# Kernel tuning notes

Hardware: AMD Instinct MI355X
Metric: run time of the kernel (lower is better)

The kernel has to match this reference:

```python
import jax, jax.numpy as jnp
import numpy as np
from jax import lax

# 4D convolution via lax.conv_general_dilated (supports N spatial dims natively)
# Layout: x is (N, C, T, U, V, W); weight is (O, I, kT, kU, kV, kW)

def conv4d(x, w, b):
    dn = lax.conv_dimension_numbers(x.shape, w.shape, ('NCTUVW', 'OITUVW', 'NCTUVW'))
    y = lax.conv_general_dilated(x, w, window_strides=(1, 1, 1, 1), padding='SAME',
                                 dimension_numbers=dn)
    return y + b[None, :, None, None, None, None]


def setup_inputs() -> dict:
    key = jax.random.key(0)
    k0, k1, k2, k3, k4 = jax.random.split(key, 5)
    B, C_in, C_hid, C_out = 2, 64, 128, 64
    T, D, H, W = 4, 16, 32, 32
    K = 3  # kernel size per dim (stmode 'C' -> (3,3,3,3))
    x = jax.random.normal(k0, (B, C_in, T, D, H, W), dtype=jnp.float32)
    scale1 = 1.0 / np.sqrt(C_in * K ** 4)
    scale2 = 1.0 / np.sqrt(C_hid * K ** 4)
    w1 = jax.random.normal(k1, (C_hid, C_in, K, K, K, K), dtype=jnp.float32) * scale1
    b1 = jax.random.normal(k2, (C_hid,), dtype=jnp.float32) * scale1
    w2 = jax.random.normal(k3, (C_out, C_hid, K, K, K, K), dtype=jnp.float32) * scale2
    b2 = jax.random.normal(k4, (C_out,), dtype=jnp.float32) * scale2
    return {"x": x, "w1": w1, "b1": b1, "w2": w2, "b2": b2}


def reference(x, w1, b1, w2, b2):
    # conv1 -> ReLU -> (dropout p=0 is identity) -> conv2 -> (dropout identity)
    h = jax.nn.relu(conv4d(x, w1, b1))
    return conv4d(h, w2, b2)
```

## Files before the change

### kernel.cpp

```cpp
#include <hip/hip_runtime.h>


using bf16x8 = __attribute__((ext_vector_type(8))) __bf16;
using f32x16 = __attribute__((ext_vector_type(16))) float;
using f32x4  = __attribute__((ext_vector_type(4))) float;

typedef __attribute__((address_space(1))) const void as1_void;
typedef __attribute__((address_space(3))) void as3_void;
__device__ __forceinline__ void gload_lds16(const void* g, void* l) {
    __builtin_amdgcn_global_load_lds((as1_void*)g, (as3_void*)l, 16, 0, 0);
}

__global__ __launch_bounds__(256) void cvt_x(const float* __restrict__ x,
                                             __bf16* __restrict__ x_t) {
    __shared__ float lt[64][65];
    const int nb = blockIdx.y;
    const int p0 = blockIdx.x * 64;
    const int tu = p0 >> 10;
    const float* src = x + (size_t)nb * 64 * 65536;
    __bf16* dst = x_t + (size_t)nb * 65536 * 64;
    #pragma unroll
    for (int i = 0; i < 16; ++i) {
        int idx = i * 256 + threadIdx.x;
        int c = idx >> 6, p = idx & 63;
        lt[c][p] = src[(size_t)c * 65536 + p0 + p];
    }
    __syncthreads();
    #pragma unroll
    for (int i = 0; i < 16; ++i) {
        int idx = i * 256 + threadIdx.x;
        int c = idx >> 6, pl = idx & 63;
        int p = p0 + pl;
        int v = (p >> 5) & 31, w = p & 31;
        dst[(size_t)(tu * 32 + v) * 2048 + (c >> 3) * 256 + w * 8 + (c & 7)] =
            (__bf16)lt[c][pl];
    }
}

template <int CIN>
__global__ __launch_bounds__(256) void cvt_w(const float* __restrict__ w,
                                             __bf16* __restrict__ wt) {
    constexpr int COUT = 8192 / CIN;
    constexpr int LOGC = (CIN == 64) ? 7 : 6;
    const int tap = blockIdx.x;
    __bf16* dst = wt + (size_t)tap * 8192;
    #pragma unroll
    for (int it = 0; it < 32; ++it) {
        const int i  = it * 256 + threadIdx.x;
        const int cl = i & 15;
        const int o  = (i >> 4) & (COUT - 1);
        const int kg = i >> (4 + LOGC);
        dst[i] = (__bf16)w[(size_t)(o * CIN + kg * 16 + cl) * 81 + tap];
    }
}

template <int CIN, int COUT, int GM, int GN, int WPEU, bool RELU>
__global__ __launch_bounds__(256, WPEU) void conv4d_mfma(
    const __bf16* __restrict__ in_t,
    const __bf16* __restrict__ wt,
    const float* __restrict__ bias,
    __bf16* __restrict__ out_bf,
    float* __restrict__ out_f)
{
    constexpr int KST   = CIN / 16;
    constexpr int UNITS = CIN / 32;
    constexpr int LOGU  = (UNITS == 2) ? 1 : 2;
    constexpr int VSPAN = GM * 4;
    constexpr int VGB   = (VSPAN == 4) ? 3 : 2;
    constexpr int ROWS  = VSPAN + 2;
    constexpr int SLOTS = ROWS * 136;
    constexpr int RNDS  = (SLOTS + 255) / 256;
    constexpr int BUFB  = SLOTS * 16;

    __shared__ __bf16 tile[2 * SLOTS * 8];

    const int tid  = threadIdx.x;
    const int lane = tid & 63;
    const int l31  = lane & 31;
    const int hl   = lane >> 5;
    const int wv   = tid >> 6;
    const int gmi  = (GM == 2) ? (wv >> 1) : 0;
    const int gni  = (GM == 2) ? (wv & 1) : wv;

    const int bid = blockIdx.x;
    const int xcd = bid & 7;
    const int s0  = bid >> 3;
    const int u   = xcd * 2 + (s0 & 1);
    const int vg  = (s0 >> 1) & ((1 << VGB) - 1);
    const int t   = (s0 >> (1 + VGB)) & 3;
    const int nb  = (s0 >> (3 + VGB)) & 1;
    const int v0  = vg * VSPAN;
    const int pbase = ((t * 16 + u) * 32 + v0) * 32;

    const __bf16* inb = in_t + (size_t)nb * 65536 * CIN;

    int goff[RNDS];
    #pragma unroll
    for (int r = 0; r < RNDS; ++r) {
        const int slot = r * 256 + tid;
        const int row  = slot / 136;
        const int rem  = slot - row * 136;
        const int chunk = rem / 34;
        const int wp   = rem - chunk * 34;
        const int v_in = v0 - 1 + row;
        const int w_in = wp - 1;
        const bool ok = (slot < SLOTS) && ((unsigned)v_in < 32u) &&
                        ((unsigned)w_in < 32u);
        goff[r] = ok ? (v_in * (CIN * 32) + chunk * 256 + w_in * 8) : -1;
    }

    #pragma unroll
    for (int r = 0; r < RNDS; ++r) {
        const int slot = r * 256 + tid;
        if (slot < SLOTS && goff[r] < 0) {
            *(uint4*)((char*)tile + slot * 16) = make_uint4(0u, 0u, 0u, 0u);
            *(uint4*)((char*)tile + BUFB + slot * 16) = make_uint4(0u, 0u, 0u, 0u);
        }
    }

    const int lane_base = gmi * 4 * 136 + hl * 34 + l31;
    const bf16x8* tile16 = (const bf16x8*)tile;

    const __bf16* wlane = wt + ((size_t)(gni * 32 + l31)) * 16 + hl * 8;

    int sb[9], tb0[9], nst = 0;
    #pragma unroll
    for (int kt = 0; kt < 3; ++kt) {
        const int t_in = t + kt - 1;
        if ((unsigned)t_in >= 4u) continue;
        #pragma unroll
        for (int ku = 0; ku < 3; ++ku) {
            const int u_in = u + ku - 1;
            if ((unsigned)u_in >= 16u) continue;
            sb[nst]  = (t_in * 16 + u_in) * 1024 * CIN;
            tb0[nst] = (kt * 3 + ku) * 9;
            ++nst;
        }
    }
    const int U = nst * UNITS;

    f32x16 acc[4];
    #pragma unroll
    for (int mt = 0; mt < 4; ++mt)
        #pragma unroll
        for (int i = 0; i < 16; ++i)
            acc[mt][i] = 0.f;

    auto issue = [&](int j) {
        const int st = j >> LOGU, ch = j & (UNITS - 1);
        const __bf16* gb = inb + sb[st] + ch * 1024;
        char* lb = ((char*)tile) + (j & 1) * BUFB + wv * 1024;
        #pragma unroll
        for (int r = 0; r < RNDS; ++r)
            if (goff[r] >= 0)
                gload_lds16(gb + goff[r], lb + r * 4096);
    };

    issue(0);
    #pragma unroll 1
    for (int i = 0; i < U; ++i) {
        asm volatile("s_waitcnt vmcnt(0) lgkmcnt(0)" ::: "memory");
        __syncthreads();
        if (i + 1 < U) issue(i + 1);

        const int st = i >> LOGU, ch = i & (UNITS - 1);
        const int tapb = tb0[st];
        const bf16x8* tb = tile16 + (i & 1) * SLOTS + lane_base;
        #pragma unroll
        for (int ks = 0; ks < 2; ++ks) {
            const int ksg = ch * 2 + ks;
            #pragma unroll
            for (int kw = 0; kw < 3; ++kw) {
                bf16x8 af[6];
                #pragma unroll
                for (int j = 0; j < 6; ++j)
                    af[j] = tb[j * 136 + ks * 68 + kw];
                bf16x8 bv[3];
                #pragma unroll
                for (int kv = 0; kv < 3; ++kv) {
                    const int wo = ((tapb + kv * 3 + kw) * KST + ksg) * (COUT * 16);
                    bv[kv] = *(const bf16x8*)(wlane + wo);
                }
                #pragma unroll
                for (int kv = 0; kv < 3; ++kv)
                    #pragma unroll
                    for (int rr = 0; rr < 4; ++rr)
                        acc[rr] = __builtin_amdgcn_mfma_f32_32x32x16_bf16(
                            af[rr + kv], bv[kv], acc[rr], 0, 0, 0);
            }
        }
    }

    {
        const int o = gni * 32 + l31;
        const float bvls = bias[o];
        #pragma unroll
        for (int rr = 0; rr < 4; ++rr) {
            const int pb = pbase + (gmi * 4 + rr) * 32;
            if constexpr (RELU) {
                #pragma unroll
                for (int rg = 0; rg < 4; ++rg)
                    #pragma unroll
                    for (int j = 0; j < 4; ++j) {
                        float v = acc[rr][rg * 4 + j] + bvls;
                        v = v > 0.f ? v : 0.f;
                        const int p = pb + j + 8 * rg + 4 * hl;
                        const int vv = (p >> 5) & 31, ww = p & 31, tu = p >> 10;
                        out_bf[(size_t)nb * 65536 * COUT +
                               (size_t)(tu * 32 + vv) * (32 * COUT) +
                               (o >> 3) * 256 + ww * 8 + (o & 7)] = (__bf16)v;
                    }
            } else {
                #pragma unroll
                for (int rg = 0; rg < 4; ++rg) {
                    f32x4 sv;
                    #pragma unroll
                    for (int j = 0; j < 4; ++j)
                        sv[j] = acc[rr][rg * 4 + j] + bvls;
                    const int p = pb + 8 * rg + 4 * hl;
                    *(f32x4*)(out_f + ((size_t)nb * COUT + o) * 65536 + p) = sv;
                }
            }
        }
    }
}

extern "C" void kernel_launch(void* const* d_in, const int* in_sizes, int n_in,
                              void* d_out, int out_size, void* d_ws, size_t ws_size,
                              hipStream_t stream) {
    const float* x  = (const float*)d_in[0];
    const float* w1 = (const float*)d_in[1];
    const float* b1 = (const float*)d_in[2];
    const float* w2 = (const float*)d_in[3];
    const float* b2 = (const float*)d_in[4];
    float* out = (float*)d_out;

    char* ws = (char*)d_ws;
    __bf16* x_t = (__bf16*)ws;
    __bf16* h_t = (__bf16*)(ws + 16777216);
    __bf16* w1t = (__bf16*)(ws + 50331648);
    __bf16* w2t = (__bf16*)(ws + 51658752);

    cvt_x<<<dim3(1024, 2), 256, 0, stream>>>(x, x_t);
    cvt_w<64><<<81, 256, 0, stream>>>(w1, w1t);
    cvt_w<128><<<81, 256, 0, stream>>>(w2, w2t);

    conv4d_mfma<64, 128, 1, 4, 3, true><<<1024, 256, 0, stream>>>(x_t, w1t, b1, h_t,
                                                                  nullptr);
    conv4d_mfma<128, 64, 2, 2, 2, false><<<512, 256, 0, stream>>>(h_t, w2t, b2,
                                                                  nullptr, out);
}
```

Measured before the change: 397.0 us.

## Software-pipeline MFMA operand loads, resplit conv2 grid, simplify input conversion

Double-buffers the LDS A-fragment and global weight loads across the six (ks,kw) groups so that the next group's operands are fetched while the current group's MFMAs run. Conv2 changes from 512 blocks of 4 waves (2x2 M/N split) to 1024 blocks of 2 waves, each covering a 4-row tile, which gives more blocks but less weight reuse per block. The input transpose kernel drops the LDS staging and has each thread gather 8 channels directly and write one vector. Global-to-LDS loads use a nontemporal cache hint and the final fp32 output uses nontemporal stores. The changes aim to hide load latency and raise occupancy, at the cost of more registers per thread and less coalesced reads in the transpose.

```diff
diff --git a/kernel.cpp b/kernel.cpp
--- a/kernel.cpp
+++ b/kernel.cpp
@@ -7,34 +7,25 @@
 
 typedef __attribute__((address_space(1))) const void as1_void;
 typedef __attribute__((address_space(3))) void as3_void;
-__device__ __forceinline__ void gload_lds16(const void* g, void* l) {
-    __builtin_amdgcn_global_load_lds((as1_void*)g, (as3_void*)l, 16, 0, 0);
+__device__ __forceinline__ void gload_lds16_nt(const void* g, void* l) {
+    __builtin_amdgcn_global_load_lds((as1_void*)g, (as3_void*)l, 16, 0, 2);
 }
 
 __global__ __launch_bounds__(256) void cvt_x(const float* __restrict__ x,
                                              __bf16* __restrict__ x_t) {
-    __shared__ float lt[64][65];
-    const int nb = blockIdx.y;
-    const int p0 = blockIdx.x * 64;
-    const int tu = p0 >> 10;
-    const float* src = x + (size_t)nb * 64 * 65536;
-    __bf16* dst = x_t + (size_t)nb * 65536 * 64;
-    #pragma unroll
-    for (int i = 0; i < 16; ++i) {
-        int idx = i * 256 + threadIdx.x;
-        int c = idx >> 6, p = idx & 63;
-        lt[c][p] = src[(size_t)c * 65536 + p0 + p];
-    }
-    __syncthreads();
-    #pragma unroll
-    for (int i = 0; i < 16; ++i) {
-        int idx = i * 256 + threadIdx.x;
-        int c = idx >> 6, pl = idx & 63;
-        int p = p0 + pl;
-        int v = (p >> 5) & 31, w = p & 31;
-        dst[(size_t)(tu * 32 + v) * 2048 + (c >> 3) * 256 + w * 8 + (c & 7)] =
-            (__bf16)lt[c][pl];
-    }
+    const int idx = blockIdx.x * 256 + threadIdx.x;
+    const int w  = idx & 31;
+    const int g  = (idx >> 5) & 7;
+    const int v  = (idx >> 8) & 31;
+    const int tu = (idx >> 13) & 63;
+    const int nb = idx >> 19;
+    const int p  = tu * 1024 + v * 32 + w;
+    const float* src = x + ((size_t)(nb * 64 + g * 8)) * 65536 + p;
+    bf16x8 o;
+    #pragma unroll
+    for (int j = 0; j < 8; ++j)
+        o[j] = (__bf16)src[(size_t)j * 65536];
+    *(bf16x8*)(x_t + (size_t)(nb * 2048 + tu * 32 + v) * 2048 + g * 256 + w * 8) = o;
 }
 
 template <int CIN>
@@ -54,23 +45,21 @@
     }
 }
 
-template <int CIN, int COUT, int GM, int GN, int WPEU, bool RELU>
-__global__ __launch_bounds__(256, WPEU) void conv4d_mfma(
+template <int CIN, int COUT, int WAVES, bool RELU>
+__global__ __launch_bounds__(WAVES * 64, 3) void conv4d_mfma(
     const __bf16* __restrict__ in_t,
     const __bf16* __restrict__ wt,
     const float* __restrict__ bias,
     __bf16* __restrict__ out_bf,
     float* __restrict__ out_f)
 {
-    constexpr int KST   = CIN / 16;
-    constexpr int UNITS = CIN / 32;
-    constexpr int LOGU  = (UNITS == 2) ? 1 : 2;
-    constexpr int VSPAN = GM * 4;
-    constexpr int VGB   = (VSPAN == 4) ? 3 : 2;
-    constexpr int ROWS  = VSPAN + 2;
-    constexpr int SLOTS = ROWS * 136;
-    constexpr int RNDS  = (SLOTS + 255) / 256;
-    constexpr int BUFB  = SLOTS * 16;
+    constexpr int KST     = CIN / 16;
+    constexpr int UNITS   = CIN / 32;
+    constexpr int LOGU    = (UNITS == 2) ? 1 : 2;
+    constexpr int THREADS = WAVES * 64;
+    constexpr int SLOTS   = 6 * 136;
+    constexpr int RNDS    = (SLOTS + THREADS - 1) / THREADS;
+    constexpr int BUFB    = SLOTS * 16;
 
     __shared__ __bf16 tile[2 * SLOTS * 8];
 
@@ -79,17 +68,16 @@
     const int l31  = lane & 31;
     const int hl   = lane >> 5;
     const int wv   = tid >> 6;
-    const int gmi  = (GM == 2) ? (wv >> 1) : 0;
-    const int gni  = (GM == 2) ? (wv & 1) : wv;
+    const int gni  = wv;
 
     const int bid = blockIdx.x;
     const int xcd = bid & 7;
     const int s0  = bid >> 3;
     const int u   = xcd * 2 + (s0 & 1);
-    const int vg  = (s0 >> 1) & ((1 << VGB) - 1);
-    const int t   = (s0 >> (1 + VGB)) & 3;
-    const int nb  = (s0 >> (3 + VGB)) & 1;
-    const int v0  = vg * VSPAN;
+    const int vg  = (s0 >> 1) & 7;
+    const int t   = (s0 >> 4) & 3;
+    const int nb  = (s0 >> 6) & 1;
+    const int v0  = vg * 4;
     const int pbase = ((t * 16 + u) * 32 + v0) * 32;
 
     const __bf16* inb = in_t + (size_t)nb * 65536 * CIN;
@@ -97,7 +85,7 @@
     int goff[RNDS];
     #pragma unroll
     for (int r = 0; r < RNDS; ++r) {
-        const int slot = r * 256 + tid;
+        const int slot = r * THREADS + tid;
         const int row  = slot / 136;
         const int rem  = slot - row * 136;
         const int chunk = rem / 34;
@@ -111,14 +99,14 @@
 
     #pragma unroll
     for (int r = 0; r < RNDS; ++r) {
-        const int slot = r * 256 + tid;
+        const int slot = r * THREADS + tid;
         if (slot < SLOTS && goff[r] < 0) {
             *(uint4*)((char*)tile + slot * 16) = make_uint4(0u, 0u, 0u, 0u);
             *(uint4*)((char*)tile + BUFB + slot * 16) = make_uint4(0u, 0u, 0u, 0u);
         }
     }
 
-    const int lane_base = gmi * 4 * 136 + hl * 34 + l31;
+    const int lane_base = hl * 34 + l31;
     const bf16x8* tile16 = (const bf16x8*)tile;
 
     const __bf16* wlane = wt + ((size_t)(gni * 32 + l31)) * 16 + hl * 8;
@@ -153,7 +141,7 @@
         #pragma unroll
         for (int r = 0; r < RNDS; ++r)
             if (goff[r] >= 0)
-                gload_lds16(gb + goff[r], lb + r * 4096);
+                gload_lds16_nt(gb + goff[r], lb + r * (THREADS * 16));
     };
 
     issue(0);
@@ -166,28 +154,34 @@
         const int st = i >> LOGU, ch = i & (UNITS - 1);
         const int tapb = tb0[st];
         const bf16x8* tb = tile16 + (i & 1) * SLOTS + lane_base;
-        #pragma unroll
-        for (int ks = 0; ks < 2; ++ks) {
-            const int ksg = ch * 2 + ks;
+
+        bf16x8 af[2][6], bv[2][3];
+        #pragma unroll
+        for (int j = 0; j < 6; ++j) af[0][j] = tb[j * 136];
+        #pragma unroll
+        for (int kv = 0; kv < 3; ++kv)
+            bv[0][kv] = *(const bf16x8*)(wlane +
+                        ((tapb + kv * 3) * KST + ch * 2) * (COUT * 16));
+
+        #pragma unroll
+        for (int g = 0; g < 6; ++g) {
+            const int cur = g & 1, nxt = cur ^ 1;
+            if (g < 5) {
+                const int gn = g + 1, ksn = gn / 3, kwn = gn % 3;
+                #pragma unroll
+                for (int j = 0; j < 6; ++j)
+                    af[nxt][j] = tb[j * 136 + ksn * 68 + kwn];
+                #pragma unroll
+                for (int kv = 0; kv < 3; ++kv)
+                    bv[nxt][kv] = *(const bf16x8*)(wlane +
+                        ((tapb + kv * 3 + kwn) * KST + ch * 2 + ksn) * (COUT * 16));
+            }
             #pragma unroll
-            for (int kw = 0; kw < 3; ++kw) {
-                bf16x8 af[6];
-                #pragma unroll
-                for (int j = 0; j < 6; ++j)
-                    af[j] = tb[j * 136 + ks * 68 + kw];
-                bf16x8 bv[3];
-                #pragma unroll
-                for (int kv = 0; kv < 3; ++kv) {
-                    const int wo = ((tapb + kv * 3 + kw) * KST + ksg) * (COUT * 16);
-                    bv[kv] = *(const bf16x8*)(wlane + wo);
-                }
-                #pragma unroll
-                for (int kv = 0; kv < 3; ++kv)
-                    #pragma unroll
-                    for (int rr = 0; rr < 4; ++rr)
-                        acc[rr] = __builtin_amdgcn_mfma_f32_32x32x16_bf16(
-                            af[rr + kv], bv[kv], acc[rr], 0, 0, 0);
-            }
+            for (int kv = 0; kv < 3; ++kv)
+                #pragma unroll
+                for (int rr = 0; rr < 4; ++rr)
+                    acc[rr] = __builtin_amdgcn_mfma_f32_32x32x16_bf16(
+                        af[cur][rr + kv], bv[cur][kv], acc[rr], 0, 0, 0);
         }
     }
 
@@ -196,7 +190,7 @@
         const float bvls = bias[o];
         #pragma unroll
         for (int rr = 0; rr < 4; ++rr) {
-            const int pb = pbase + (gmi * 4 + rr) * 32;
+            const int pb = pbase + rr * 32;
             if constexpr (RELU) {
                 #pragma unroll
                 for (int rg = 0; rg < 4; ++rg)
@@ -218,7 +212,8 @@
                     for (int j = 0; j < 4; ++j)
                         sv[j] = acc[rr][rg * 4 + j] + bvls;
                     const int p = pb + 8 * rg + 4 * hl;
-                    *(f32x4*)(out_f + ((size_t)nb * COUT + o) * 65536 + p) = sv;
+                    __builtin_nontemporal_store(sv,
+                        (f32x4*)(out_f + ((size_t)nb * COUT + o) * 65536 + p));
                 }
             }
         }
@@ -241,12 +236,12 @@
     __bf16* w1t = (__bf16*)(ws + 50331648);
     __bf16* w2t = (__bf16*)(ws + 51658752);
 
-    cvt_x<<<dim3(1024, 2), 256, 0, stream>>>(x, x_t);
+    cvt_x<<<4096, 256, 0, stream>>>(x, x_t);
     cvt_w<64><<<81, 256, 0, stream>>>(w1, w1t);
     cvt_w<128><<<81, 256, 0, stream>>>(w2, w2t);
 
-    conv4d_mfma<64, 128, 1, 4, 3, true><<<1024, 256, 0, stream>>>(x_t, w1t, b1, h_t,
-                                                                  nullptr);
-    conv4d_mfma<128, 64, 2, 2, 2, false><<<512, 256, 0, stream>>>(h_t, w2t, b2,
-                                                                  nullptr, out);
-}
+    conv4d_mfma<64, 128, 4, true><<<1024, 256, 0, stream>>>(x_t, w1t, b1, h_t,
+                                                            nullptr);
+    conv4d_mfma<128, 64, 2, false><<<1024, 128, 0, stream>>>(h_t, w2t, b2, nullptr,
+                                                             out);
+}
```

Result: no change. 400.1 us (+0.8%).
